# Kernel optimization log

Measured on AMD Instinct MI355X. Metric: run time of the kernel, lower is better.

Reference implementation:

```python
import jax, jax.numpy as jnp
import numpy as np

N = 100000   # nodes
E = 1600000  # edges
H = 256      # hidden_dim
G = 64       # graphs in batch
OUT = 2      # out_dim


def setup_inputs() -> dict:
    key = jax.random.key(0)
    ks = jax.random.split(key, 20)
    f32 = jnp.float32

    def w(k, shape, fan_in):
        lim = 1.0 / np.sqrt(fan_in)
        return jax.random.uniform(k, shape, f32, -lim, lim)

    return {
        "content_x": jax.random.normal(ks[0], (N, 310), f32),
        "bert_x":    jax.random.normal(ks[1], (N, 768), f32),
        "profile_x": jax.random.normal(ks[2], (N, 10), f32),
        "spacy_x":   jax.random.normal(ks[3], (N, 300), f32),
        "edge_index": jax.random.randint(ks[4], (2, E), 0, N, dtype=jnp.int32),
        "batch":      jax.random.randint(ks[5], (N,), 0, G, dtype=jnp.int32),
        # feature-branch linears
        "Wc": w(ks[6], (310, H), 310), "bc": jnp.zeros((H,), f32),
        "Wb": w(ks[7], (768, H), 768), "bb": jnp.zeros((H,), f32),
        "Wp": w(ks[8], (10, H), 10),   "bp": jnp.zeros((H,), f32),
        "Ws": w(ks[9], (300, H), 300), "bs": jnp.zeros((H,), f32),
        # GCN conv weights (PyG GCNConv: x @ W, aggregate, + bias)
        "Wg1": w(ks[10], (4 * H, H), 4 * H), "bg1": jnp.zeros((H,), f32),
        "Wg2": w(ks[11], (H, H), H),         "bg2": jnp.zeros((H,), f32),
        # head linears
        "Wl1": w(ks[12], (H, H), H),   "bl1": jnp.zeros((H,), f32),
        "Wl2": w(ks[13], (H, OUT), H), "bl2": jnp.zeros((OUT,), f32),
    }


def gcn_conv(x, W, b, src, dst, n_nodes):
    """PyG GCNConv with added self-loops and symmetric normalization."""
    h = x @ W  # [N, out]
    # degree (dst side) including self-loop
    deg = jnp.ones((n_nodes,), h.dtype).at[dst].add(1.0)
    dinv = jax.lax.rsqrt(deg)
    coef = (dinv[src] * dinv[dst])[:, None]          # [E,1]
    agg = jax.ops.segment_sum(h[src] * coef, dst, num_segments=n_nodes)
    agg = agg + h * (dinv * dinv)[:, None]           # self-loop term
    return agg + b


def reference(content_x, bert_x, profile_x, spacy_x, edge_index, batch,
              Wc, bc, Wb, bb, Wp, bp, Ws, bs,
              Wg1, bg1, Wg2, bg2, Wl1, bl1, Wl2, bl2):
    relu = jax.nn.relu
    # multi-branch linear + relu, then concat
    out = jnp.concatenate([
        relu(content_x @ Wc + bc),
        relu(bert_x @ Wb + bb),
        relu(profile_x @ Wp + bp),
        relu(spacy_x @ Ws + bs),
    ], axis=1)  # [N, 4H]
    # dropout is identity at inference
    src, dst = edge_index[0], edge_index[1]
    out = relu(gcn_conv(out, Wg1, bg1, src, dst, N))
    out = relu(gcn_conv(out, Wg2, bg2, src, dst, N))
    # global mean pool over graphs
    ones = jnp.ones((N,), out.dtype)
    cnt = jax.ops.segment_sum(ones, batch, num_segments=G)
    pooled = jax.ops.segment_sum(out, batch, num_segments=G)
    pooled = pooled / jnp.maximum(cnt, 1.0)[:, None]  # [G, H]
    h = relu(pooled @ Wl1 + bl1)
    logits = h @ Wl2 + bl2
    return jax.nn.log_softmax(logits, axis=-1)
```

## Files before the change

### kernel.cpp

```cpp
#include <hip/hip_runtime.h>
#include <hip/hip_bf16.h>
#include <stdint.h>

#define NN 100000
#define NE 1600000
#define HID 256
#define NGRAPH 64
#define POOL_BLOCKS 256

typedef __attribute__((ext_vector_type(8))) short short8;
typedef __attribute__((ext_vector_type(4))) float f32x4;
typedef __attribute__((ext_vector_type(4))) unsigned int u32x4;

static __device__ inline float bf2f(unsigned short u){
  union { unsigned int i; float f; } x; x.i = ((unsigned int)u) << 16; return x.f;
}
static __device__ inline unsigned short f2bf(float f){
  union { float f; unsigned int i; } x; x.f = f;
  unsigned int r = x.i + 0x7fffu + ((x.i >> 16) & 1u);
  return (unsigned short)(r >> 16);
}

static __device__ inline void gload16(const void* g, void* l){
  __builtin_amdgcn_global_load_lds((const __attribute__((address_space(1))) void*)g,
                                   (__attribute__((address_space(3))) void*)l, 16, 0, 0);
}

template<bool F32A>
__global__ __launch_bounds__(512) void gemm_k(
    const void* __restrict__ Aq, int lda, int K, int Kp,
    const unsigned short* __restrict__ WT,
    const float* __restrict__ bias,
    unsigned short* __restrict__ C, int ldc, int M, int relu)
{
  __shared__ unsigned char smem[49152];
  const int tid  = threadIdx.x;
  const int lane = tid & 63;
  const int wid  = tid >> 6;
  const int wm   = wid >> 2;
  const int wn   = wid & 3;
  const int bm   = blockIdx.x * 128;
  const int l15  = lane & 15;
  const int lk   = lane >> 4;

  f32x4 acc[4][4];
#pragma unroll
  for (int i = 0; i < 4; i++)
#pragma unroll
    for (int j = 0; j < 4; j++) acc[i][j] = (f32x4){0.f, 0.f, 0.f, 0.f};

  for (int k0 = 0; k0 < Kp; k0 += 64) {
    __syncthreads();
    if (F32A) {
      const float* A = (const float*)Aq;
#pragma unroll
      for (int it = 0; it < 2; ++it) {
        int chunk = it * 512 + tid;
        int row = chunk >> 3;
        int c   = chunk & 7;
        int gr  = bm + row; if (gr >= M) gr = M - 1;
        int cg  = c ^ (row & 7);
        int kb  = k0 + cg * 8;
        const float* ap = A + (size_t)gr * lda;
        u32x4 pk;
#pragma unroll
        for (int hh = 0; hh < 4; ++hh) {
          int ka = kb + 2 * hh, kc = kb + 2 * hh + 1;
          float v0 = (ka < K) ? ap[ka] : 0.f;
          float v1 = (kc < K) ? ap[kc] : 0.f;
          pk[hh] = (unsigned int)f2bf(v0) | ((unsigned int)f2bf(v1) << 16);
        }
        *(u32x4*)(smem + row * 128 + c * 16) = pk;
      }
    } else {
      const unsigned short* A = (const unsigned short*)Aq;
#pragma unroll
      for (int it = 0; it < 2; ++it) {
        int inst = wid * 2 + it;
        int row  = inst * 8 + (lane >> 3);
        int c    = lane & 7;
        int gr   = bm + row; if (gr >= M) gr = M - 1;
        int cg   = c ^ (row & 7);
        gload16(A + (size_t)gr * lda + k0 + cg * 8, smem + inst * 1024);
      }
    }
#pragma unroll
    for (int it = 0; it < 4; ++it) {
      int inst = wid * 4 + it;
      int nr   = inst * 8 + (lane >> 3);
      int c    = lane & 7;
      int cg   = c ^ (nr & 7);
      gload16(WT + (size_t)nr * Kp + k0 + cg * 8, smem + 16384 + inst * 1024);
    }
    __syncthreads();

#pragma unroll
    for (int s2 = 0; s2 < 2; ++s2) {
      short8 a[4], b[4];
#pragma unroll
      for (int i = 0; i < 4; i++) {
        int row = wm * 64 + i * 16 + l15;
        int ch  = (s2 * 4 + lk) ^ (row & 7);
        a[i] = *(const short8*)(smem + row * 128 + ch * 16);
      }
#pragma unroll
      for (int j = 0; j < 4; j++) {
        int col = wn * 64 + j * 16 + l15;
        int ch  = (s2 * 4 + lk) ^ (col & 7);
        b[j] = *(const short8*)(smem + 16384 + col * 128 + ch * 16);
      }
#pragma unroll
      for (int i = 0; i < 4; i++)
#pragma unroll
        for (int j = 0; j < 4; j++)
          acc[i][j] = __builtin_amdgcn_mfma_f32_16x16x32_bf16(a[i], b[j], acc[i][j], 0, 0, 0);
    }
  }

#pragma unroll
  for (int j = 0; j < 4; j++) {
    int col = wn * 64 + j * 16 + l15;
    float bv = bias ? bias[col] : 0.f;
#pragma unroll
    for (int i = 0; i < 4; i++) {
#pragma unroll
      for (int r = 0; r < 4; r++) {
        int row = bm + wm * 64 + i * 16 + lk * 4 + r;
        if (row < M) {
          float v = acc[i][j][r] + bv;
          if (relu) v = fmaxf(v, 0.f);
          C[(size_t)row * ldc + col] = f2bf(v);
        }
      }
    }
  }
}

__global__ void wconv_k(const float* __restrict__ W, unsigned short* __restrict__ WT,
                        int K, int Kp)
{
  int idx = blockIdx.x * 256 + threadIdx.x;
  if (idx >= 256 * Kp) return;
  int n = idx / Kp, k = idx - n * Kp;
  float v = (k < K) ? W[(size_t)k * 256 + n] : 0.f;
  WT[(size_t)n * Kp + k] = f2bf(v);
}

__global__ void zero_int_k(int* p, int n){
  int i = blockIdx.x * 256 + threadIdx.x; if (i < n) p[i] = 0;
}
__global__ void count_k(const int* __restrict__ dst, int* __restrict__ cnt, int n){
  int e = blockIdx.x * 256 + threadIdx.x; if (e < n) atomicAdd(&cnt[dst[e]], 1);
}
__global__ void deg_k(const int* __restrict__ cnt, float* __restrict__ dinv,
                      float* __restrict__ selfc, int n){
  int i = blockIdx.x * 256 + threadIdx.x;
  if (i < n) { float d = 1.0f + (float)cnt[i]; dinv[i] = rsqrtf(d); selfc[i] = 1.0f / d; }
}
__global__ void scan1_k(const int* __restrict__ cnt, int* __restrict__ bsum, int n){
  __shared__ int s[256];
  int b = blockIdx.x, t = threadIdx.x;
  int base = b * 1024 + t * 4, v = 0;
#pragma unroll
  for (int j = 0; j < 4; j++) { int i = base + j; if (i < n) v += cnt[i]; }
  s[t] = v; __syncthreads();
  for (int o = 128; o > 0; o >>= 1) { if (t < o) s[t] += s[t + o]; __syncthreads(); }
  if (t == 0) bsum[b] = s[0];
}
__global__ void scan2_k(int* bsum, int nb){
  __shared__ int s[256];
  int t = threadIdx.x;
  int v = (t < nb) ? bsum[t] : 0;
  s[t] = v; __syncthreads();
  for (int o = 1; o < 256; o <<= 1) {
    int x = (t >= o) ? s[t - o] : 0; __syncthreads();
    s[t] += x; __syncthreads();
  }
  if (t < nb) bsum[t] = s[t] - v;
}
__global__ void scan3_k(const int* __restrict__ cnt, const int* __restrict__ bsum,
                        int* __restrict__ rowstart, int* __restrict__ cursor, int n){
  __shared__ int s[256];
  int b = blockIdx.x, t = threadIdx.x;
  int base = b * 1024 + t * 4;
  int c0 = 0, c1 = 0, c2 = 0, c3 = 0;
  if (base + 0 < n) c0 = cnt[base + 0];
  if (base + 1 < n) c1 = cnt[base + 1];
  if (base + 2 < n) c2 = cnt[base + 2];
  if (base + 3 < n) c3 = cnt[base + 3];
  int ts = c0 + c1 + c2 + c3;
  s[t] = ts; __syncthreads();
  for (int o = 1; o < 256; o <<= 1) {
    int x = (t >= o) ? s[t - o] : 0; __syncthreads();
    s[t] += x; __syncthreads();
  }
  int run = bsum[b] + s[t] - ts;
  int cc[4] = {c0, c1, c2, c3};
#pragma unroll
  for (int j = 0; j < 4; j++) {
    int i = base + j;
    if (i < n) {
      rowstart[i] = run; cursor[i] = run; run += cc[j];
      if (i == n - 1) rowstart[n] = run;
    }
  }
}
__global__ void scatter_k(const int* __restrict__ src, const int* __restrict__ dst,
                          const float* __restrict__ dinv, int* __restrict__ cursor,
                          int* __restrict__ csr_src, float* __restrict__ csr_coef, int n){
  int e = blockIdx.x * 256 + threadIdx.x; if (e >= n) return;
  int d = dst[e], s = src[e];
  int p = atomicAdd(&cursor[d], 1);
  csr_src[p] = s;
  csr_coef[p] = dinv[s] * dinv[d];
}

__global__ __launch_bounds__(256) void agg_k(
    const unsigned short* __restrict__ h,
    const int* __restrict__ rowstart, const int* __restrict__ csr_src,
    const float* __restrict__ csr_coef, const float* __restrict__ selfc,
    const float* __restrict__ bias, unsigned short* __restrict__ out)
{
  int dst = blockIdx.x * 4 + (threadIdx.x >> 6);
  if (dst >= NN) return;
  int lane = threadIdx.x & 63;
  int colb = lane * 4;
  ushort4 hv = *(const ushort4*)(h + (size_t)dst * 256 + colb);
  float sc = selfc[dst];
  float a0 = sc * bf2f(hv.x), a1 = sc * bf2f(hv.y), a2 = sc * bf2f(hv.z), a3 = sc * bf2f(hv.w);
  int e0 = rowstart[dst], e1 = rowstart[dst + 1];
  int e = e0;
  for (; e + 1 < e1; e += 2) {
    int s0 = csr_src[e], s1 = csr_src[e + 1];
    float cf0 = csr_coef[e], cf1 = csr_coef[e + 1];
    ushort4 v0 = *(const ushort4*)(h + (size_t)s0 * 256 + colb);
    ushort4 v1 = *(const ushort4*)(h + (size_t)s1 * 256 + colb);
    a0 += cf0 * bf2f(v0.x); a1 += cf0 * bf2f(v0.y); a2 += cf0 * bf2f(v0.z); a3 += cf0 * bf2f(v0.w);
    a0 += cf1 * bf2f(v1.x); a1 += cf1 * bf2f(v1.y); a2 += cf1 * bf2f(v1.z); a3 += cf1 * bf2f(v1.w);
  }
  if (e < e1) {
    int s0 = csr_src[e]; float cf0 = csr_coef[e];
    ushort4 v0 = *(const ushort4*)(h + (size_t)s0 * 256 + colb);
    a0 += cf0 * bf2f(v0.x); a1 += cf0 * bf2f(v0.y); a2 += cf0 * bf2f(v0.z); a3 += cf0 * bf2f(v0.w);
  }
  float4 bv = *(const float4*)(bias + colb);
  a0 = fmaxf(a0 + bv.x, 0.f); a1 = fmaxf(a1 + bv.y, 0.f);
  a2 = fmaxf(a2 + bv.z, 0.f); a3 = fmaxf(a3 + bv.w, 0.f);
  ushort4 o; o.x = f2bf(a0); o.y = f2bf(a1); o.z = f2bf(a2); o.w = f2bf(a3);
  *(ushort4*)(out + (size_t)dst * 256 + colb) = o;
}

__global__ __launch_bounds__(256) void pool_k(
    const unsigned short* __restrict__ x, const int* __restrict__ batch,
    float* __restrict__ pp, float* __restrict__ cp)
{
  __shared__ float acc[NGRAPH][HID];
  __shared__ float cl[NGRAPH];
  int t = threadIdx.x, b = blockIdx.x;
  for (int i = t; i < NGRAPH * HID; i += 256) ((float*)acc)[i] = 0.f;
  if (t < NGRAPH) cl[t] = 0.f;
  __syncthreads();
  int per = (NN + POOL_BLOCKS - 1) / POOL_BLOCKS;
  int i0 = b * per, i1 = min(NN, i0 + per);
  for (int i = i0; i < i1; ++i) {
    int g = batch[i];
    acc[g][t] += bf2f(x[(size_t)i * 256 + t]);
    if (t == 0) cl[g] += 1.f;
  }
  __syncthreads();
  for (int g = 0; g < NGRAPH; ++g) pp[(size_t)b * (NGRAPH * HID) + g * HID + t] = acc[g][t];
  if (t < NGRAPH) cp[b * NGRAPH + t] = cl[t];
}

__global__ __launch_bounds__(256) void head_k(
    const float* __restrict__ pp, const float* __restrict__ cp,
    const float* __restrict__ Wl1, const float* __restrict__ bl1,
    const float* __restrict__ Wl2, const float* __restrict__ bl2,
    float* __restrict__ out)
{
  __shared__ float pooled[HID];
  __shared__ float red[2][4];
  int g = blockIdx.x, t = threadIdx.x;
  float s = 0.f;
  for (int b = 0; b < POOL_BLOCKS; ++b) s += pp[(size_t)b * (NGRAPH * HID) + g * HID + t];
  float cnt = 0.f;
  for (int b = 0; b < POOL_BLOCKS; ++b) cnt += cp[b * NGRAPH + g];
  pooled[t] = s / fmaxf(cnt, 1.f);
  __syncthreads();
  float hv = bl1[t];
  for (int k = 0; k < HID; ++k) hv += pooled[k] * Wl1[k * HID + t];
  hv = fmaxf(hv, 0.f);
  float p0 = hv * Wl2[t * 2 + 0];
  float p1 = hv * Wl2[t * 2 + 1];
  for (int o = 32; o > 0; o >>= 1) { p0 += __shfl_down(p0, o); p1 += __shfl_down(p1, o); }
  int w = t >> 6;
  if ((t & 63) == 0) { red[0][w] = p0; red[1][w] = p1; }
  __syncthreads();
  if (t == 0) {
    float l0 = bl2[0], l1 = bl2[1];
#pragma unroll
    for (int i = 0; i < 4; i++) { l0 += red[0][i]; l1 += red[1][i]; }
    float m = fmaxf(l0, l1);
    float lse = m + logf(expf(l0 - m) + expf(l1 - m));
    out[g * 2 + 0] = l0 - lse;
    out[g * 2 + 1] = l1 - lse;
  }
}

extern "C" void kernel_launch(void* const* d_in, const int* in_sizes, int n_in,
                              void* d_out, int out_size, void* d_ws, size_t ws_size,
                              hipStream_t stream)
{
  const float* content = (const float*)d_in[0];
  const float* bert    = (const float*)d_in[1];
  const float* profile = (const float*)d_in[2];
  const float* spacy   = (const float*)d_in[3];
  const int*   eidx    = (const int*)d_in[4];
  const int*   batch   = (const int*)d_in[5];
  const float* Wc = (const float*)d_in[6];  const float* bc = (const float*)d_in[7];
  const float* Wb = (const float*)d_in[8];  const float* bb = (const float*)d_in[9];
  const float* Wp = (const float*)d_in[10]; const float* bp = (const float*)d_in[11];
  const float* Ws = (const float*)d_in[12]; const float* bs = (const float*)d_in[13];
  const float* Wg1 = (const float*)d_in[14]; const float* bg1 = (const float*)d_in[15];
  const float* Wg2 = (const float*)d_in[16]; const float* bg2 = (const float*)d_in[17];
  const float* Wl1 = (const float*)d_in[18]; const float* bl1 = (const float*)d_in[19];
  const float* Wl2 = (const float*)d_in[20]; const float* bl2 = (const float*)d_in[21];
  float* out = (float*)d_out;
  const int* srcp = eidx;
  const int* dstp = eidx + NE;

  const int KPC = 320, KPB = 768, KPP = 64, KPS = 320, KPG1 = 1024, KPG2 = 256;

  char* ws = (char*)d_ws;
  size_t off = 0;
  auto alloc = [&](size_t bytes) { size_t o = off; off += (bytes + 255) & ~(size_t)255; return o; };

  unsigned short* WTc  = (unsigned short*)(ws + alloc((size_t)256 * KPC * 2));
  unsigned short* WTb  = (unsigned short*)(ws + alloc((size_t)256 * KPB * 2));
  unsigned short* WTp  = (unsigned short*)(ws + alloc((size_t)256 * KPP * 2));
  unsigned short* WTs  = (unsigned short*)(ws + alloc((size_t)256 * KPS * 2));
  unsigned short* WTg1 = (unsigned short*)(ws + alloc((size_t)256 * KPG1 * 2));
  unsigned short* WTg2 = (unsigned short*)(ws + alloc((size_t)256 * KPG2 * 2));
  float* dinv    = (float*)(ws + alloc((size_t)NN * 4));
  float* selfc   = (float*)(ws + alloc((size_t)NN * 4));
  int* rowcnt    = (int*)(ws + alloc((size_t)NN * 4));
  int* rowstart  = (int*)(ws + alloc((size_t)(NN + 1) * 4));
  int* cursor    = (int*)(ws + alloc((size_t)NN * 4));
  int* csr_src   = (int*)(ws + alloc((size_t)NE * 4));
  float* csr_coef= (float*)(ws + alloc((size_t)NE * 4));
  int* bsum      = (int*)(ws + alloc(1024));
  float* pp      = (float*)(ws + alloc((size_t)POOL_BLOCKS * NGRAPH * HID * 4));
  float* cp      = (float*)(ws + alloc((size_t)POOL_BLOCKS * NGRAPH * 4));
  unsigned short* X1 = (unsigned short*)(ws + alloc((size_t)NN * 1024 * 2));
  unsigned short* H  = (unsigned short*)(ws + alloc((size_t)NN * 256 * 2));
  unsigned short* X2 = (unsigned short*)(ws + alloc((size_t)NN * 256 * 2));
  unsigned short* X3 = (unsigned short*)(ws + alloc((size_t)NN * 256 * 2));
  (void)ws_size; (void)in_sizes; (void)n_in; (void)out_size;

  hipStream_t s = stream;
  const int NB = (NN + 1023) / 1024;
  const int GEMM_GRID = (NN + 127) / 128;

  wconv_k<<<(256 * KPC + 255) / 256, 256, 0, s>>>(Wc, WTc, 310, KPC);
  wconv_k<<<(256 * KPB + 255) / 256, 256, 0, s>>>(Wb, WTb, 768, KPB);
  wconv_k<<<(256 * KPP + 255) / 256, 256, 0, s>>>(Wp, WTp, 10, KPP);
  wconv_k<<<(256 * KPS + 255) / 256, 256, 0, s>>>(Ws, WTs, 300, KPS);
  wconv_k<<<(256 * KPG1 + 255) / 256, 256, 0, s>>>(Wg1, WTg1, 1024, KPG1);
  wconv_k<<<(256 * KPG2 + 255) / 256, 256, 0, s>>>(Wg2, WTg2, 256, KPG2);

  zero_int_k<<<(NN + 255) / 256, 256, 0, s>>>(rowcnt, NN);
  count_k<<<(NE + 255) / 256, 256, 0, s>>>(dstp, rowcnt, NE);
  deg_k<<<(NN + 255) / 256, 256, 0, s>>>(rowcnt, dinv, selfc, NN);
  scan1_k<<<NB, 256, 0, s>>>(rowcnt, bsum, NN);
  scan2_k<<<1, 256, 0, s>>>(bsum, NB);
  scan3_k<<<NB, 256, 0, s>>>(rowcnt, bsum, rowstart, cursor, NN);
  scatter_k<<<(NE + 255) / 256, 256, 0, s>>>(srcp, dstp, dinv, cursor, csr_src, csr_coef, NE);

  gemm_k<true><<<GEMM_GRID, 512, 0, s>>>(content, 310, 310, KPC, WTc, bc, X1 + 0,   1024, NN, 1);
  gemm_k<true><<<GEMM_GRID, 512, 0, s>>>(bert,    768, 768, KPB, WTb, bb, X1 + 256, 1024, NN, 1);
  gemm_k<true><<<GEMM_GRID, 512, 0, s>>>(profile, 10,  10,  KPP, WTp, bp, X1 + 512, 1024, NN, 1);
  gemm_k<true><<<GEMM_GRID, 512, 0, s>>>(spacy,   300, 300, KPS, WTs, bs, X1 + 768, 1024, NN, 1);

  gemm_k<false><<<GEMM_GRID, 512, 0, s>>>(X1, 1024, 1024, KPG1, WTg1, nullptr, H, 256, NN, 0);
  agg_k<<<(NN + 3) / 4, 256, 0, s>>>(H, rowstart, csr_src, csr_coef, selfc, bg1, X2);

  gemm_k<false><<<GEMM_GRID, 512, 0, s>>>(X2, 256, 256, KPG2, WTg2, nullptr, H, 256, NN, 0);
  agg_k<<<(NN + 3) / 4, 256, 0, s>>>(H, rowstart, csr_src, csr_coef, selfc, bg2, X3);

  pool_k<<<POOL_BLOCKS, 256, 0, s>>>(X3, batch, pp, cp);
  head_k<<<NGRAPH, 256, 0, s>>>(pp, cp, Wl1, bl1, Wl2, bl2, out);
}
```

Measured before the change: 1.628 ms.

## Double-buffer GEMM with 128x128 tiles, batch branch GEMMs, unroll aggregation

Replaces the single-buffered 128x256 GEMM (512 threads, K-step 64) with a double-buffered 128x128 tile GEMM (256 threads, K-step 32). The next K slice is prefetched while MFMAs run on the current one, and f32 inputs are loaded with vector loads and packed after compute. The four feature-branch GEMMs now run as one launch using blockIdx.z, and the profile branch's K padding shrinks from 64 to 32. Aggregation unrolls to four edges per iteration for more memory-level parallelism. The smaller N tile means the A operand is loaded twice, once per column block.

```diff
diff --git a/kernel.cpp b/kernel.cpp
--- a/kernel.cpp
+++ b/kernel.cpp
@@ -10,6 +10,7 @@
 
 typedef __attribute__((ext_vector_type(8))) short short8;
 typedef __attribute__((ext_vector_type(4))) float f32x4;
+typedef __attribute__((ext_vector_type(2))) float f32x2;
 typedef __attribute__((ext_vector_type(4))) unsigned int u32x4;
 
 static __device__ inline float bf2f(unsigned short u){
@@ -20,28 +21,69 @@
   unsigned int r = x.i + 0x7fffu + ((x.i >> 16) & 1u);
   return (unsigned short)(r >> 16);
 }
-
 static __device__ inline void gload16(const void* g, void* l){
   __builtin_amdgcn_global_load_lds((const __attribute__((address_space(1))) void*)g,
                                    (__attribute__((address_space(3))) void*)l, 16, 0, 0);
 }
 
-template<bool F32A>
-__global__ __launch_bounds__(512) void gemm_k(
-    const void* __restrict__ Aq, int lda, int K, int Kp,
-    const unsigned short* __restrict__ WT,
-    const float* __restrict__ bias,
-    unsigned short* __restrict__ C, int ldc, int M, int relu)
-{
-  __shared__ unsigned char smem[49152];
+struct GArgs {
+  const void* A;
+  const unsigned short* WT;
+  const float* bias;
+  unsigned short* C;
+  int lda, K, Kp, ldc;
+};
+
+template<bool F32A, bool RELU>
+__global__ __launch_bounds__(256) void gemm2_k(GArgs g0, GArgs g1, GArgs g2, GArgs g3, int M)
+{
+  __shared__ unsigned char smem[2][16384];
+  GArgs g = g0;
+  if (blockIdx.z == 1) g = g1;
+  else if (blockIdx.z == 2) g = g2;
+  else if (blockIdx.z == 3) g = g3;
+
   const int tid  = threadIdx.x;
   const int lane = tid & 63;
   const int wid  = tid >> 6;
-  const int wm   = wid >> 2;
-  const int wn   = wid & 3;
+  const int wm   = wid >> 1;
+  const int wn   = wid & 1;
   const int bm   = blockIdx.x * 128;
+  const int bn   = blockIdx.y * 128;
   const int l15  = lane & 15;
   const int lk   = lane >> 4;
+  const int K    = g.K;
+  const int lda  = g.lda;
+  const int Kp   = g.Kp;
+  const int NK   = Kp >> 5;
+
+  int rowB[2], coB[2];
+#pragma unroll
+  for (int it = 0; it < 2; ++it) {
+    int cidx = it * 256 + wid * 64 + lane;
+    int row = cidx >> 2, ce = cidx & 3;
+    rowB[it] = row;
+    coB[it]  = (ce ^ ((row >> 1) & 3)) * 8;
+  }
+  int grA[2], coA[2];
+#pragma unroll
+  for (int it = 0; it < 2; ++it) {
+    int cidx = it * 256 + wid * 64 + lane;
+    int row = cidx >> 2, ce = cidx & 3;
+    int gr = bm + row; if (gr >= M) gr = M - 1;
+    grA[it] = gr;
+    coA[it] = (ce ^ ((row >> 1) & 3)) * 8;
+  }
+  int grF[2], kcF[2], wbF[2];
+#pragma unroll
+  for (int it = 0; it < 2; ++it) {
+    int cidx = it * 256 + tid;
+    int row = cidx >> 2, c = cidx & 3;
+    int gr = bm + row; if (gr >= M) gr = M - 1;
+    grF[it] = gr;
+    kcF[it] = c * 8;
+    wbF[it] = row * 64 + ((c ^ ((row >> 1) & 3)) << 4);
+  }
 
   f32x4 acc[4][4];
 #pragma unroll
@@ -49,78 +91,98 @@
 #pragma unroll
     for (int j = 0; j < 4; j++) acc[i][j] = (f32x4){0.f, 0.f, 0.f, 0.f};
 
-  for (int k0 = 0; k0 < Kp; k0 += 64) {
+  const unsigned short* Ab = (const unsigned short*)g.A;
+  const float* Af = (const float*)g.A;
+
+  float fv[2][8];
+
+#define STAGE_B(buf, k0_) do { \
+  _Pragma("unroll") \
+  for (int it = 0; it < 2; ++it) \
+    gload16(g.WT + (size_t)(bn + rowB[it]) * Kp + (k0_) + coB[it], \
+            &smem[buf][8192 + (it * 256 + wid * 64) * 16]); \
+} while (0)
+
+#define STAGE_A16(buf, k0_) do { \
+  _Pragma("unroll") \
+  for (int it = 0; it < 2; ++it) \
+    gload16(Ab + (size_t)grA[it] * lda + (k0_) + coA[it], \
+            &smem[buf][(it * 256 + wid * 64) * 16]); \
+} while (0)
+
+#define LOAD_F32(k0_) do { \
+  if ((k0_) + 32 <= K) { \
+    _Pragma("unroll") \
+    for (int it = 0; it < 2; ++it) { \
+      const float* bp = Af + (size_t)grF[it] * lda + (k0_) + kcF[it]; \
+      _Pragma("unroll") \
+      for (int q = 0; q < 4; ++q) { \
+        f32x2 v = *(const f32x2*)(bp + 2 * q); \
+        fv[it][2 * q] = v.x; fv[it][2 * q + 1] = v.y; \
+      } \
+    } \
+  } else { \
+    _Pragma("unroll") \
+    for (int it = 0; it < 2; ++it) { \
+      const float* bp = Af + (size_t)grF[it] * lda; \
+      _Pragma("unroll") \
+      for (int h = 0; h < 8; ++h) { \
+        int k = (k0_) + kcF[it] + h; \
+        fv[it][h] = (k < K) ? bp[k] : 0.f; \
+      } \
+    } \
+  } \
+} while (0)
+
+#define WRITE_F32(buf) do { \
+  _Pragma("unroll") \
+  for (int it = 0; it < 2; ++it) { \
+    u32x4 pk; \
+    _Pragma("unroll") \
+    for (int q = 0; q < 4; ++q) \
+      pk[q] = (unsigned int)f2bf(fv[it][2 * q]) | ((unsigned int)f2bf(fv[it][2 * q + 1]) << 16); \
+    *(u32x4*)(&smem[buf][wbF[it]]) = pk; \
+  } \
+} while (0)
+
+  if (F32A) { LOAD_F32(0); WRITE_F32(0); }
+  else      { STAGE_A16(0, 0); }
+  STAGE_B(0, 0);
+  __syncthreads();
+
+  for (int ks = 0; ks < NK; ++ks) {
+    const int cur = ks & 1;
+    const int k0n = (ks + 1) << 5;
+    const bool havenext = (ks + 1 < NK);
+    if (havenext) {
+      if (F32A) LOAD_F32(k0n);
+      else      STAGE_A16(cur ^ 1, k0n);
+      STAGE_B(cur ^ 1, k0n);
+    }
+    short8 a[4], b[4];
+#pragma unroll
+    for (int i = 0; i < 4; i++) {
+      int row = wm * 64 + i * 16 + l15;
+      a[i] = *(const short8*)(&smem[cur][row * 64 + ((lk ^ ((row >> 1) & 3)) << 4)]);
+    }
+#pragma unroll
+    for (int j = 0; j < 4; j++) {
+      int row = wn * 64 + j * 16 + l15;
+      b[j] = *(const short8*)(&smem[cur][8192 + row * 64 + ((lk ^ ((row >> 1) & 3)) << 4)]);
+    }
+#pragma unroll
+    for (int i = 0; i < 4; i++)
+#pragma unroll
+      for (int j = 0; j < 4; j++)
+        acc[i][j] = __builtin_amdgcn_mfma_f32_16x16x32_bf16(a[i], b[j], acc[i][j], 0, 0, 0);
+    if (F32A && havenext) WRITE_F32(cur ^ 1);
     __syncthreads();
-    if (F32A) {
-      const float* A = (const float*)Aq;
-#pragma unroll
-      for (int it = 0; it < 2; ++it) {
-        int chunk = it * 512 + tid;
-        int row = chunk >> 3;
-        int c   = chunk & 7;
-        int gr  = bm + row; if (gr >= M) gr = M - 1;
-        int cg  = c ^ (row & 7);
-        int kb  = k0 + cg * 8;
-        const float* ap = A + (size_t)gr * lda;
-        u32x4 pk;
-#pragma unroll
-        for (int hh = 0; hh < 4; ++hh) {
-          int ka = kb + 2 * hh, kc = kb + 2 * hh + 1;
-          float v0 = (ka < K) ? ap[ka] : 0.f;
-          float v1 = (kc < K) ? ap[kc] : 0.f;
-          pk[hh] = (unsigned int)f2bf(v0) | ((unsigned int)f2bf(v1) << 16);
-        }
-        *(u32x4*)(smem + row * 128 + c * 16) = pk;
-      }
-    } else {
-      const unsigned short* A = (const unsigned short*)Aq;
-#pragma unroll
-      for (int it = 0; it < 2; ++it) {
-        int inst = wid * 2 + it;
-        int row  = inst * 8 + (lane >> 3);
-        int c    = lane & 7;
-        int gr   = bm + row; if (gr >= M) gr = M - 1;
-        int cg   = c ^ (row & 7);
-        gload16(A + (size_t)gr * lda + k0 + cg * 8, smem + inst * 1024);
-      }
-    }
-#pragma unroll
-    for (int it = 0; it < 4; ++it) {
-      int inst = wid * 4 + it;
-      int nr   = inst * 8 + (lane >> 3);
-      int c    = lane & 7;
-      int cg   = c ^ (nr & 7);
-      gload16(WT + (size_t)nr * Kp + k0 + cg * 8, smem + 16384 + inst * 1024);
-    }
-    __syncthreads();
-
-#pragma unroll
-    for (int s2 = 0; s2 < 2; ++s2) {
-      short8 a[4], b[4];
-#pragma unroll
-      for (int i = 0; i < 4; i++) {
-        int row = wm * 64 + i * 16 + l15;
-        int ch  = (s2 * 4 + lk) ^ (row & 7);
-        a[i] = *(const short8*)(smem + row * 128 + ch * 16);
-      }
-#pragma unroll
-      for (int j = 0; j < 4; j++) {
-        int col = wn * 64 + j * 16 + l15;
-        int ch  = (s2 * 4 + lk) ^ (col & 7);
-        b[j] = *(const short8*)(smem + 16384 + col * 128 + ch * 16);
-      }
-#pragma unroll
-      for (int i = 0; i < 4; i++)
-#pragma unroll
-        for (int j = 0; j < 4; j++)
-          acc[i][j] = __builtin_amdgcn_mfma_f32_16x16x32_bf16(a[i], b[j], acc[i][j], 0, 0, 0);
-    }
   }
 
 #pragma unroll
   for (int j = 0; j < 4; j++) {
-    int col = wn * 64 + j * 16 + l15;
-    float bv = bias ? bias[col] : 0.f;
+    int col = bn + wn * 64 + j * 16 + l15;
+    float bv = g.bias ? g.bias[col] : 0.f;
 #pragma unroll
     for (int i = 0; i < 4; i++) {
 #pragma unroll
@@ -128,12 +190,16 @@
         int row = bm + wm * 64 + i * 16 + lk * 4 + r;
         if (row < M) {
           float v = acc[i][j][r] + bv;
-          if (relu) v = fmaxf(v, 0.f);
-          C[(size_t)row * ldc + col] = f2bf(v);
+          if (RELU) v = fmaxf(v, 0.f);
+          g.C[(size_t)row * g.ldc + col] = f2bf(v);
         }
       }
     }
   }
+#undef STAGE_B
+#undef STAGE_A16
+#undef LOAD_F32
+#undef WRITE_F32
 }
 
 __global__ void wconv_k(const float* __restrict__ W, unsigned short* __restrict__ WT,
@@ -225,23 +291,28 @@
   if (dst >= NN) return;
   int lane = threadIdx.x & 63;
   int colb = lane * 4;
-  ushort4 hv = *(const ushort4*)(h + (size_t)dst * 256 + colb);
+  const unsigned short* hb = h + colb;
+  ushort4 hv = *(const ushort4*)(hb + (size_t)dst * 256);
   float sc = selfc[dst];
   float a0 = sc * bf2f(hv.x), a1 = sc * bf2f(hv.y), a2 = sc * bf2f(hv.z), a3 = sc * bf2f(hv.w);
   int e0 = rowstart[dst], e1 = rowstart[dst + 1];
   int e = e0;
-  for (; e + 1 < e1; e += 2) {
-    int s0 = csr_src[e], s1 = csr_src[e + 1];
-    float cf0 = csr_coef[e], cf1 = csr_coef[e + 1];
-    ushort4 v0 = *(const ushort4*)(h + (size_t)s0 * 256 + colb);
-    ushort4 v1 = *(const ushort4*)(h + (size_t)s1 * 256 + colb);
-    a0 += cf0 * bf2f(v0.x); a1 += cf0 * bf2f(v0.y); a2 += cf0 * bf2f(v0.z); a3 += cf0 * bf2f(v0.w);
-    a0 += cf1 * bf2f(v1.x); a1 += cf1 * bf2f(v1.y); a2 += cf1 * bf2f(v1.z); a3 += cf1 * bf2f(v1.w);
-  }
-  if (e < e1) {
-    int s0 = csr_src[e]; float cf0 = csr_coef[e];
-    ushort4 v0 = *(const ushort4*)(h + (size_t)s0 * 256 + colb);
-    a0 += cf0 * bf2f(v0.x); a1 += cf0 * bf2f(v0.y); a2 += cf0 * bf2f(v0.z); a3 += cf0 * bf2f(v0.w);
+  for (; e + 4 <= e1; e += 4) {
+    int s0 = csr_src[e], s1 = csr_src[e + 1], s2 = csr_src[e + 2], s3 = csr_src[e + 3];
+    float c0 = csr_coef[e], c1 = csr_coef[e + 1], c2 = csr_coef[e + 2], c3 = csr_coef[e + 3];
+    ushort4 v0 = *(const ushort4*)(hb + (size_t)s0 * 256);
+    ushort4 v1 = *(const ushort4*)(hb + (size_t)s1 * 256);
+    ushort4 v2 = *(const ushort4*)(hb + (size_t)s2 * 256);
+    ushort4 v3 = *(const ushort4*)(hb + (size_t)s3 * 256);
+    a0 += c0 * bf2f(v0.x) + c1 * bf2f(v1.x) + c2 * bf2f(v2.x) + c3 * bf2f(v3.x);
+    a1 += c0 * bf2f(v0.y) + c1 * bf2f(v1.y) + c2 * bf2f(v2.y) + c3 * bf2f(v3.y);
+    a2 += c0 * bf2f(v0.z) + c1 * bf2f(v1.z) + c2 * bf2f(v2.z) + c3 * bf2f(v3.z);
+    a3 += c0 * bf2f(v0.w) + c1 * bf2f(v1.w) + c2 * bf2f(v2.w) + c3 * bf2f(v3.w);
+  }
+  for (; e < e1; ++e) {
+    int s0 = csr_src[e]; float c0 = csr_coef[e];
+    ushort4 v0 = *(const ushort4*)(hb + (size_t)s0 * 256);
+    a0 += c0 * bf2f(v0.x); a1 += c0 * bf2f(v0.y); a2 += c0 * bf2f(v0.z); a3 += c0 * bf2f(v0.w);
   }
   float4 bv = *(const float4*)(bias + colb);
   a0 = fmaxf(a0 + bv.x, 0.f); a1 = fmaxf(a1 + bv.y, 0.f);
@@ -329,7 +400,7 @@
   const int* srcp = eidx;
   const int* dstp = eidx + NE;
 
-  const int KPC = 320, KPB = 768, KPP = 64, KPS = 320, KPG1 = 1024, KPG2 = 256;
+  const int KPC = 320, KPB = 768, KPP = 32, KPS = 320, KPG1 = 1024, KPG2 = 256;
 
   char* ws = (char*)d_ws;
   size_t off = 0;
@@ -359,7 +430,7 @@
 
   hipStream_t s = stream;
   const int NB = (NN + 1023) / 1024;
-  const int GEMM_GRID = (NN + 127) / 128;
+  const int MB = (NN + 127) / 128;
 
   wconv_k<<<(256 * KPC + 255) / 256, 256, 0, s>>>(Wc, WTc, 310, KPC);
   wconv_k<<<(256 * KPB + 255) / 256, 256, 0, s>>>(Wb, WTb, 768, KPB);
@@ -376,15 +447,24 @@
   scan3_k<<<NB, 256, 0, s>>>(rowcnt, bsum, rowstart, cursor, NN);
   scatter_k<<<(NE + 255) / 256, 256, 0, s>>>(srcp, dstp, dinv, cursor, csr_src, csr_coef, NE);
 
-  gemm_k<true><<<GEMM_GRID, 512, 0, s>>>(content, 310, 310, KPC, WTc, bc, X1 + 0,   1024, NN, 1);
-  gemm_k<true><<<GEMM_GRID, 512, 0, s>>>(bert,    768, 768, KPB, WTb, bb, X1 + 256, 1024, NN, 1);
-  gemm_k<true><<<GEMM_GRID, 512, 0, s>>>(profile, 10,  10,  KPP, WTp, bp, X1 + 512, 1024, NN, 1);
-  gemm_k<true><<<GEMM_GRID, 512, 0, s>>>(spacy,   300, 300, KPS, WTs, bs, X1 + 768, 1024, NN, 1);
-
-  gemm_k<false><<<GEMM_GRID, 512, 0, s>>>(X1, 1024, 1024, KPG1, WTg1, nullptr, H, 256, NN, 0);
+  {
+    GArgs gc = { content, WTc, bc, X1 + 0,   310, 310, KPC, 1024 };
+    GArgs gb = { bert,    WTb, bb, X1 + 256, 768, 768, KPB, 1024 };
+    GArgs gp = { profile, WTp, bp, X1 + 512, 10,  10,  KPP, 1024 };
+    GArgs gs = { spacy,   WTs, bs, X1 + 768, 300, 300, KPS, 1024 };
+    gemm2_k<true, true><<<dim3(MB, 2, 4), 256, 0, s>>>(gc, gb, gp, gs, NN);
+  }
+
+  {
+    GArgs g1 = { X1, WTg1, nullptr, H, 1024, 1024, KPG1, 256 };
+    gemm2_k<false, false><<<dim3(MB, 2, 1), 256, 0, s>>>(g1, g1, g1, g1, NN);
+  }
   agg_k<<<(NN + 3) / 4, 256, 0, s>>>(H, rowstart, csr_src, csr_coef, selfc, bg1, X2);
 
-  gemm_k<false><<<GEMM_GRID, 512, 0, s>>>(X2, 256, 256, KPG2, WTg2, nullptr, H, 256, NN, 0);
+  {
+    GArgs g2 = { X2, WTg2, nullptr, H, 256, 256, KPG2, 256 };
+    gemm2_k<false, false><<<dim3(MB, 2, 1), 256, 0, s>>>(g2, g2, g2, g2, NN);
+  }
   agg_k<<<(NN + 3) / 4, 256, 0, s>>>(H, rowstart, csr_src, csr_coef, selfc, bg2, X3);
 
   pool_k<<<POOL_BLOCKS, 256, 0, s>>>(X3, batch, pp, cp);
```

After: 1.610 ms. Within noise of the previous version (-1.1%).

## Pipeline GEMM loads with multi-buffered LDS and fuse branch GEMMs into one launch

Applied to the files above, without the earlier changes.

Replaces the single-stage GEMM with software-pipelined kernels. The fp32-input kernel prefetches the next K-slice into registers and converts it while MFMAs run on a double-buffered LDS tile. The bf16 kernel triple-buffers direct global-to-LDS loads using explicit vmcnt waits. Tiles shrink to 128x128 with 256 threads and a 2D grid over N, the four branch GEMMs merge into one launch via blockIdx.z, output stores are packed in pairs through a lane shuffle, and the aggregation loop is unrolled by 8 so more gathers are in flight. The hand-coded waitcnt counts must match the number of outstanding loads; if they do not, the kernel risks races.

```diff
diff --git a/kernel.cpp b/kernel.cpp
--- a/kernel.cpp
+++ b/kernel.cpp
@@ -20,120 +20,223 @@
   unsigned int r = x.i + 0x7fffu + ((x.i >> 16) & 1u);
   return (unsigned short)(r >> 16);
 }
-
 static __device__ inline void gload16(const void* g, void* l){
   __builtin_amdgcn_global_load_lds((const __attribute__((address_space(1))) void*)g,
                                    (__attribute__((address_space(3))) void*)l, 16, 0, 0);
 }
-
-template<bool F32A>
-__global__ __launch_bounds__(512) void gemm_k(
-    const void* __restrict__ Aq, int lda, int K, int Kp,
-    const unsigned short* __restrict__ WT,
-    const float* __restrict__ bias,
-    unsigned short* __restrict__ C, int ldc, int M, int relu)
-{
-  __shared__ unsigned char smem[49152];
-  const int tid  = threadIdx.x;
-  const int lane = tid & 63;
-  const int wid  = tid >> 6;
-  const int wm   = wid >> 2;
-  const int wn   = wid & 3;
-  const int bm   = blockIdx.x * 128;
-  const int l15  = lane & 15;
-  const int lk   = lane >> 4;
-
+static __device__ __forceinline__ void fence_bar_v8(){
+  asm volatile("s_waitcnt vmcnt(8) lgkmcnt(0)" ::: "memory");
+  __builtin_amdgcn_s_barrier(); __builtin_amdgcn_sched_barrier(0);
+}
+static __device__ __forceinline__ void fence_bar_v4(){
+  asm volatile("s_waitcnt vmcnt(4) lgkmcnt(0)" ::: "memory");
+  __builtin_amdgcn_s_barrier(); __builtin_amdgcn_sched_barrier(0);
+}
+static __device__ __forceinline__ void fence_bar_v0(){
+  asm volatile("s_waitcnt vmcnt(0) lgkmcnt(0)" ::: "memory");
+  __builtin_amdgcn_s_barrier(); __builtin_amdgcn_sched_barrier(0);
+}
+
+struct GArgs {
+  const void* A;
+  const unsigned short* WT;
+  const float* bias;
+  unsigned short* C;
+  int lda, K, Kp, ldc;
+};
+
+__global__ __launch_bounds__(256) void gemmf_k(GArgs g0, GArgs g1, GArgs g2, GArgs g3, int M)
+{
+  __shared__ unsigned char smem[2][16384];
+  GArgs g = g0;
+  if (blockIdx.z == 1) g = g1;
+  else if (blockIdx.z == 2) g = g2;
+  else if (blockIdx.z == 3) g = g3;
+
+  const int tid = threadIdx.x, lane = tid & 63, wid = tid >> 6;
+  const int wm = wid >> 1, wn = wid & 1;
+  const int bm = blockIdx.x * 128, bn = blockIdx.y * 128;
+  const int l15 = lane & 15, lk = lane >> 4;
+  const int K = g.K, Kp = g.Kp, lda = g.lda, NK = Kp >> 5;
+  const float* Af = (const float*)g.A;
+
+  size_t rbF[2]; int kcF[2], wbF[2];
+#pragma unroll
+  for (int it = 0; it < 2; ++it) {
+    int cidx = it * 256 + tid, row = cidx >> 2, c = cidx & 3;
+    int gr = bm + row; if (gr >= M) gr = M - 1;
+    rbF[it] = (size_t)gr * lda; kcF[it] = c * 8;
+    wbF[it] = row * 64 + ((c ^ ((row >> 1) & 3)) << 4);
+  }
+  size_t obB[2]; int ldsB[2];
+#pragma unroll
+  for (int it = 0; it < 2; ++it) {
+    int inst = it * 4 + wid, cidx = inst * 64 + lane, row = cidx >> 2, c = cidx & 3;
+    obB[it] = (size_t)(bn + row) * Kp + (c ^ ((row >> 1) & 3)) * 8;
+    ldsB[it] = 8192 + inst * 1024;
+  }
+
+  float2 fvA[8], fvB[8];
   f32x4 acc[4][4];
 #pragma unroll
   for (int i = 0; i < 4; i++)
 #pragma unroll
     for (int j = 0; j < 4; j++) acc[i][j] = (f32x4){0.f, 0.f, 0.f, 0.f};
 
-  for (int k0 = 0; k0 < Kp; k0 += 64) {
-    __syncthreads();
-    if (F32A) {
-      const float* A = (const float*)Aq;
-#pragma unroll
-      for (int it = 0; it < 2; ++it) {
-        int chunk = it * 512 + tid;
-        int row = chunk >> 3;
-        int c   = chunk & 7;
-        int gr  = bm + row; if (gr >= M) gr = M - 1;
-        int cg  = c ^ (row & 7);
-        int kb  = k0 + cg * 8;
-        const float* ap = A + (size_t)gr * lda;
-        u32x4 pk;
-#pragma unroll
-        for (int hh = 0; hh < 4; ++hh) {
-          int ka = kb + 2 * hh, kc = kb + 2 * hh + 1;
-          float v0 = (ka < K) ? ap[ka] : 0.f;
-          float v1 = (kc < K) ? ap[kc] : 0.f;
-          pk[hh] = (unsigned int)f2bf(v0) | ((unsigned int)f2bf(v1) << 16);
-        }
-        *(u32x4*)(smem + row * 128 + c * 16) = pk;
-      }
-    } else {
-      const unsigned short* A = (const unsigned short*)Aq;
-#pragma unroll
-      for (int it = 0; it < 2; ++it) {
-        int inst = wid * 2 + it;
-        int row  = inst * 8 + (lane >> 3);
-        int c    = lane & 7;
-        int gr   = bm + row; if (gr >= M) gr = M - 1;
-        int cg   = c ^ (row & 7);
-        gload16(A + (size_t)gr * lda + k0 + cg * 8, smem + inst * 1024);
+#define LOADF(S, k0_) do{ \
+  if ((k0_) + 32 <= K) { \
+    _Pragma("unroll") for (int it = 0; it < 2; ++it){ \
+      const float* bp = Af + rbF[it] + (k0_) + kcF[it]; \
+      _Pragma("unroll") for (int q = 0; q < 4; ++q) S[it*4+q] = *(const float2*)(bp + 2*q); \
+    } \
+  } else { \
+    _Pragma("unroll") for (int it = 0; it < 2; ++it){ \
+      const float* bp = Af + rbF[it]; \
+      _Pragma("unroll") for (int q = 0; q < 4; ++q){ \
+        int k = (k0_) + kcF[it] + 2*q; \
+        S[it*4+q].x = (k < K) ? bp[k] : 0.f; \
+        S[it*4+q].y = (k+1 < K) ? bp[k+1] : 0.f; \
+      } } } } while(0)
+
+#define CVTW(S, bufb) do{ \
+  _Pragma("unroll") for (int it = 0; it < 2; ++it){ \
+    u32x4 pk; \
+    _Pragma("unroll") for (int q = 0; q < 4; ++q) \
+      pk[q] = (unsigned)f2bf(S[it*4+q].x) | ((unsigned)f2bf(S[it*4+q].y) << 16); \
+    *(u32x4*)(&smem[bufb][wbF[it]]) = pk; } } while(0)
+
+#define STAGEB(bufb, k0_) do{ \
+  _Pragma("unroll") for (int it = 0; it < 2; ++it) \
+    gload16(g.WT + obB[it] + (k0_), &smem[bufb][ldsB[it]]); } while(0)
+
+#define DOMFMA(bufb) do{ \
+  short8 a[4], b[4]; \
+  _Pragma("unroll") for (int i = 0; i < 4; ++i){ int row = wm*64 + i*16 + l15; \
+    a[i] = *(const short8*)(&smem[bufb][row*64 + ((lk ^ ((row>>1)&3)) << 4)]); } \
+  _Pragma("unroll") for (int j = 0; j < 4; ++j){ int row = wn*64 + j*16 + l15; \
+    b[j] = *(const short8*)(&smem[bufb][8192 + row*64 + ((lk ^ ((row>>1)&3)) << 4)]); } \
+  _Pragma("unroll") for (int i = 0; i < 4; ++i) \
+    _Pragma("unroll") for (int j = 0; j < 4; ++j) \
+      acc[i][j] = __builtin_amdgcn_mfma_f32_16x16x32_bf16(a[i], b[j], acc[i][j], 0, 0, 0); \
+  } while(0)
+
+  LOADF(fvA, 0);
+  CVTW(fvA, 0);
+  STAGEB(0, 0);
+  LOADF(fvB, 32);
+  fence_bar_v8();
+
+  for (int t = 0; t < NK; t += 2) {
+    { const bool h1 = (t + 1) < NK, h2 = (t + 2) < NK;
+      if (h1) STAGEB(1, (t + 1) << 5);
+      if (h2) LOADF(fvA, (t + 2) << 5);
+      DOMFMA(0);
+      if (h1) CVTW(fvB, 1);
+      if (h2) fence_bar_v8(); else fence_bar_v0(); }
+    { const bool h1 = (t + 2) < NK, h2 = (t + 3) < NK;
+      if (h1) STAGEB(0, (t + 2) << 5);
+      if (h2) LOADF(fvB, (t + 3) << 5);
+      DOMFMA(1);
+      if (h1) CVTW(fvA, 0);
+      if (h2) fence_bar_v8(); else fence_bar_v0(); }
+  }
+
+#pragma unroll
+  for (int j = 0; j < 4; j++) {
+    int col = bn + wn * 64 + j * 16 + l15;
+    float bv = g.bias[col];
+#pragma unroll
+    for (int i = 0; i < 4; i++) {
+#pragma unroll
+      for (int r = 0; r < 4; r++) {
+        int row = bm + wm * 64 + i * 16 + lk * 4 + r;
+        float v = fmaxf(acc[i][j][r] + bv, 0.f);
+        unsigned u = f2bf(v);
+        unsigned pu = (unsigned)__shfl_xor((int)u, 1);
+        if (!(lane & 1) && row < M)
+          *(unsigned*)(g.C + (size_t)row * g.ldc + col) = u | (pu << 16);
       }
     }
-#pragma unroll
-    for (int it = 0; it < 4; ++it) {
-      int inst = wid * 4 + it;
-      int nr   = inst * 8 + (lane >> 3);
-      int c    = lane & 7;
-      int cg   = c ^ (nr & 7);
-      gload16(WT + (size_t)nr * Kp + k0 + cg * 8, smem + 16384 + inst * 1024);
-    }
-    __syncthreads();
-
-#pragma unroll
-    for (int s2 = 0; s2 < 2; ++s2) {
-      short8 a[4], b[4];
-#pragma unroll
-      for (int i = 0; i < 4; i++) {
-        int row = wm * 64 + i * 16 + l15;
-        int ch  = (s2 * 4 + lk) ^ (row & 7);
-        a[i] = *(const short8*)(smem + row * 128 + ch * 16);
-      }
-#pragma unroll
-      for (int j = 0; j < 4; j++) {
-        int col = wn * 64 + j * 16 + l15;
-        int ch  = (s2 * 4 + lk) ^ (col & 7);
-        b[j] = *(const short8*)(smem + 16384 + col * 128 + ch * 16);
-      }
-#pragma unroll
-      for (int i = 0; i < 4; i++)
-#pragma unroll
-        for (int j = 0; j < 4; j++)
-          acc[i][j] = __builtin_amdgcn_mfma_f32_16x16x32_bf16(a[i], b[j], acc[i][j], 0, 0, 0);
-    }
+  }
+#undef LOADF
+#undef CVTW
+#undef STAGEB
+#undef DOMFMA
+}
+
+__global__ __launch_bounds__(256) void gemmb_k(GArgs g, int M)
+{
+  __shared__ unsigned char smem[49152];
+  const int tid = threadIdx.x, lane = tid & 63, wid = tid >> 6;
+  const int wm = wid >> 1, wn = wid & 1;
+  const int bm = blockIdx.x * 128, bn = blockIdx.y * 128;
+  const int l15 = lane & 15, lk = lane >> 4;
+  const int Kp = g.Kp, lda = g.lda, NK = Kp >> 5;
+  const unsigned short* Ab = (const unsigned short*)g.A;
+
+  size_t obA[2], obB[2]; int ldsA[2], ldsB[2];
+#pragma unroll
+  for (int it = 0; it < 2; ++it) {
+    int inst = it * 4 + wid, cidx = inst * 64 + lane, row = cidx >> 2, c = cidx & 3;
+    int gr = bm + row; if (gr >= M) gr = M - 1;
+    obA[it] = (size_t)gr * lda + (c ^ ((row >> 1) & 3)) * 8;
+    ldsA[it] = inst * 1024;
+    obB[it] = (size_t)(bn + row) * Kp + (c ^ ((row >> 1) & 3)) * 8;
+    ldsB[it] = 8192 + inst * 1024;
+  }
+
+  f32x4 acc[4][4];
+#pragma unroll
+  for (int i = 0; i < 4; i++)
+#pragma unroll
+    for (int j = 0; j < 4; j++) acc[i][j] = (f32x4){0.f, 0.f, 0.f, 0.f};
+
+#define STAGE3(ob_, k0_) do{ \
+  _Pragma("unroll") for (int it = 0; it < 2; ++it) \
+    gload16(Ab + obA[it] + (k0_), smem + (ob_) + ldsA[it]); \
+  _Pragma("unroll") for (int it = 0; it < 2; ++it) \
+    gload16(g.WT + obB[it] + (k0_), smem + (ob_) + ldsB[it]); } while(0)
+
+  STAGE3(0, 0);
+  STAGE3(16384, 32);
+  fence_bar_v4();
+  int o0 = 0, o1 = 16384, o2 = 32768;
+
+  for (int t = 0; t < NK; ++t) {
+    const bool h2 = (t + 2) < NK;
+    if (h2) STAGE3(o2, (t + 2) << 5);
+    short8 a[4], b[4];
+#pragma unroll
+    for (int i = 0; i < 4; ++i) { int row = wm * 64 + i * 16 + l15;
+      a[i] = *(const short8*)(smem + o0 + row * 64 + ((lk ^ ((row >> 1) & 3)) << 4)); }
+#pragma unroll
+    for (int j = 0; j < 4; ++j) { int row = wn * 64 + j * 16 + l15;
+      b[j] = *(const short8*)(smem + o0 + 8192 + row * 64 + ((lk ^ ((row >> 1) & 3)) << 4)); }
+#pragma unroll
+    for (int i = 0; i < 4; ++i)
+#pragma unroll
+      for (int j = 0; j < 4; ++j)
+        acc[i][j] = __builtin_amdgcn_mfma_f32_16x16x32_bf16(a[i], b[j], acc[i][j], 0, 0, 0);
+    if (h2) fence_bar_v4(); else fence_bar_v0();
+    int tmp = o0; o0 = o1; o1 = o2; o2 = tmp;
   }
 
 #pragma unroll
   for (int j = 0; j < 4; j++) {
-    int col = wn * 64 + j * 16 + l15;
-    float bv = bias ? bias[col] : 0.f;
+    int col = bn + wn * 64 + j * 16 + l15;
 #pragma unroll
     for (int i = 0; i < 4; i++) {
 #pragma unroll
       for (int r = 0; r < 4; r++) {
         int row = bm + wm * 64 + i * 16 + lk * 4 + r;
-        if (row < M) {
-          float v = acc[i][j][r] + bv;
-          if (relu) v = fmaxf(v, 0.f);
-          C[(size_t)row * ldc + col] = f2bf(v);
-        }
+        unsigned u = f2bf(acc[i][j][r]);
+        unsigned pu = (unsigned)__shfl_xor((int)u, 1);
+        if (!(lane & 1) && row < M)
+          *(unsigned*)(g.C + (size_t)row * g.ldc + col) = u | (pu << 16);
       }
     }
   }
+#undef STAGE3
 }
 
 __global__ void wconv_k(const float* __restrict__ W, unsigned short* __restrict__ WT,
@@ -225,23 +328,36 @@
   if (dst >= NN) return;
   int lane = threadIdx.x & 63;
   int colb = lane * 4;
-  ushort4 hv = *(const ushort4*)(h + (size_t)dst * 256 + colb);
+  const unsigned short* hb = h + colb;
+  ushort4 hv = *(const ushort4*)(hb + (size_t)dst * 256);
   float sc = selfc[dst];
   float a0 = sc * bf2f(hv.x), a1 = sc * bf2f(hv.y), a2 = sc * bf2f(hv.z), a3 = sc * bf2f(hv.w);
   int e0 = rowstart[dst], e1 = rowstart[dst + 1];
   int e = e0;
-  for (; e + 1 < e1; e += 2) {
+  for (; e + 8 <= e1; e += 8) {
+    int ss[8]; float cc[8]; ushort4 vv[8];
+#pragma unroll
+    for (int q = 0; q < 8; ++q) { ss[q] = csr_src[e + q]; cc[q] = csr_coef[e + q]; }
+#pragma unroll
+    for (int q = 0; q < 8; ++q) vv[q] = *(const ushort4*)(hb + (size_t)ss[q] * 256);
+#pragma unroll
+    for (int q = 0; q < 8; ++q) {
+      a0 += cc[q] * bf2f(vv[q].x); a1 += cc[q] * bf2f(vv[q].y);
+      a2 += cc[q] * bf2f(vv[q].z); a3 += cc[q] * bf2f(vv[q].w);
+    }
+  }
+  for (; e + 2 <= e1; e += 2) {
     int s0 = csr_src[e], s1 = csr_src[e + 1];
-    float cf0 = csr_coef[e], cf1 = csr_coef[e + 1];
-    ushort4 v0 = *(const ushort4*)(h + (size_t)s0 * 256 + colb);
-    ushort4 v1 = *(const ushort4*)(h + (size_t)s1 * 256 + colb);
-    a0 += cf0 * bf2f(v0.x); a1 += cf0 * bf2f(v0.y); a2 += cf0 * bf2f(v0.z); a3 += cf0 * bf2f(v0.w);
-    a0 += cf1 * bf2f(v1.x); a1 += cf1 * bf2f(v1.y); a2 += cf1 * bf2f(v1.z); a3 += cf1 * bf2f(v1.w);
+    float c0 = csr_coef[e], c1 = csr_coef[e + 1];
+    ushort4 v0 = *(const ushort4*)(hb + (size_t)s0 * 256);
+    ushort4 v1 = *(const ushort4*)(hb + (size_t)s1 * 256);
+    a0 += c0 * bf2f(v0.x) + c1 * bf2f(v1.x); a1 += c0 * bf2f(v0.y) + c1 * bf2f(v1.y);
+    a2 += c0 * bf2f(v0.z) + c1 * bf2f(v1.z); a3 += c0 * bf2f(v0.w) + c1 * bf2f(v1.w);
   }
   if (e < e1) {
-    int s0 = csr_src[e]; float cf0 = csr_coef[e];
-    ushort4 v0 = *(const ushort4*)(h + (size_t)s0 * 256 + colb);
-    a0 += cf0 * bf2f(v0.x); a1 += cf0 * bf2f(v0.y); a2 += cf0 * bf2f(v0.z); a3 += cf0 * bf2f(v0.w);
+    int s0 = csr_src[e]; float c0 = csr_coef[e];
+    ushort4 v0 = *(const ushort4*)(hb + (size_t)s0 * 256);
+    a0 += c0 * bf2f(v0.x); a1 += c0 * bf2f(v0.y); a2 += c0 * bf2f(v0.z); a3 += c0 * bf2f(v0.w);
   }
   float4 bv = *(const float4*)(bias + colb);
   a0 = fmaxf(a0 + bv.x, 0.f); a1 = fmaxf(a1 + bv.y, 0.f);
@@ -359,7 +475,7 @@
 
   hipStream_t s = stream;
   const int NB = (NN + 1023) / 1024;
-  const int GEMM_GRID = (NN + 127) / 128;
+  const int MB = (NN + 127) / 128;
 
   wconv_k<<<(256 * KPC + 255) / 256, 256, 0, s>>>(Wc, WTc, 310, KPC);
   wconv_k<<<(256 * KPB + 255) / 256, 256, 0, s>>>(Wb, WTb, 768, KPB);
@@ -376,15 +492,24 @@
   scan3_k<<<NB, 256, 0, s>>>(rowcnt, bsum, rowstart, cursor, NN);
   scatter_k<<<(NE + 255) / 256, 256, 0, s>>>(srcp, dstp, dinv, cursor, csr_src, csr_coef, NE);
 
-  gemm_k<true><<<GEMM_GRID, 512, 0, s>>>(content, 310, 310, KPC, WTc, bc, X1 + 0,   1024, NN, 1);
-  gemm_k<true><<<GEMM_GRID, 512, 0, s>>>(bert,    768, 768, KPB, WTb, bb, X1 + 256, 1024, NN, 1);
-  gemm_k<true><<<GEMM_GRID, 512, 0, s>>>(profile, 10,  10,  KPP, WTp, bp, X1 + 512, 1024, NN, 1);
-  gemm_k<true><<<GEMM_GRID, 512, 0, s>>>(spacy,   300, 300, KPS, WTs, bs, X1 + 768, 1024, NN, 1);
-
-  gemm_k<false><<<GEMM_GRID, 512, 0, s>>>(X1, 1024, 1024, KPG1, WTg1, nullptr, H, 256, NN, 0);
+  {
+    GArgs gc = { content, WTc, bc, X1 + 0,   310, 310, KPC, 1024 };
+    GArgs gb = { bert,    WTb, bb, X1 + 256, 768, 768, KPB, 1024 };
+    GArgs gp = { profile, WTp, bp, X1 + 512, 10,  10,  KPP, 1024 };
+    GArgs gs = { spacy,   WTs, bs, X1 + 768, 300, 300, KPS, 1024 };
+    gemmf_k<<<dim3(MB, 2, 4), 256, 0, s>>>(gc, gb, gp, gs, NN);
+  }
+
+  {
+    GArgs g1 = { X1, WTg1, nullptr, H, 1024, 1024, KPG1, 256 };
+    gemmb_k<<<dim3(MB, 2, 1), 256, 0, s>>>(g1, NN);
+  }
   agg_k<<<(NN + 3) / 4, 256, 0, s>>>(H, rowstart, csr_src, csr_coef, selfc, bg1, X2);
 
-  gemm_k<false><<<GEMM_GRID, 512, 0, s>>>(X2, 256, 256, KPG2, WTg2, nullptr, H, 256, NN, 0);
+  {
+    GArgs g2 = { X2, WTg2, nullptr, H, 256, 256, KPG2, 256 };
+    gemmb_k<<<dim3(MB, 2, 1), 256, 0, s>>>(g2, NN);
+  }
   agg_k<<<(NN + 3) / 4, 256, 0, s>>>(H, rowstart, csr_src, csr_coef, selfc, bg2, X3);
 
   pool_k<<<POOL_BLOCKS, 256, 0, s>>>(X3, batch, pp, cp);
```

Result: faster. 1.544 ms (-5.2%).
